# Optimization experiments

Measured on AMD Instinct MI355X. Metric: run time of the kernel, lower is better.

The kernel has to match this reference:

```python
import jax, jax.numpy as jnp
import numpy as np

EPSILON = 0.1  # adversarial perturbation magnitude (q = 1 norm)
N_HIDDEN1 = 4096


def setup_inputs() -> dict:
    key = jax.random.key(0)
    ks = jax.random.split(key, 6)
    batch, n_in, n_hid, n_out = 4096, 2048, N_HIDDEN1, 1024
    x = jax.random.normal(ks[0], (batch, n_in), dtype=jnp.float32)
    y = jax.random.normal(ks[1], (batch, n_out), dtype=jnp.float32)
    # AdvLinearNet params: beta ~ U[0,1)/sqrt(n_out), bias = 0
    beta = jax.random.uniform(ks[2], (n_in, n_out), dtype=jnp.float32) / np.sqrt(n_out)
    bias_lin = jnp.zeros((n_out,), dtype=jnp.float32)
    # AdvOneLayer params (gamma = 1.0): W1 = -U/ (gamma*n_hid), W2 = U/(gamma*n_out)
    W1 = -jax.random.uniform(ks[3], (n_hid, n_in), dtype=jnp.float32) / n_hid
    W2 = jax.random.uniform(ks[4], (n_out, n_hid), dtype=jnp.float32) / n_out
    bias1 = jnp.zeros((n_hid,), dtype=jnp.float32)
    bias2 = jnp.zeros((n_out,), dtype=jnp.float32)
    return {"x": x, "y": y, "beta": beta, "bias_lin": bias_lin,
            "W1": W1, "W2": W2, "bias1": bias1, "bias2": bias2, "adv": 1}


def reference(x, y, beta, bias_lin, W1, W2, bias1, bias2, adv):
    # ---- AdvLinearNet ----
    lin = jnp.matmul(x, beta) + bias_lin            # [B, n_out]
    if adv:
        # torch.norm(beta, dim=0, p=1) -> per-output-column L1 norm
        beta_norm = jnp.sum(jnp.abs(beta), axis=0)  # [n_out]
        lin = lin - EPSILON * y * beta_norm
    # ---- AdvOneLayer ----
    if adv:
        # Faithful to source: summand = W2[i, j] * n_hidden1 (the relu hidden
        # computation inside the double loop is dead code), so the adv output
        # is constant across the batch.
        one = N_HIDDEN1 * jnp.sum(W2, axis=1) + bias2      # [n_out]
        one = jnp.broadcast_to(one, lin.shape)             # [B, n_out]
    else:
        h = jax.nn.relu(jnp.matmul(x, W1.T) + bias1)       # [B, n_hid]
        one = jnp.matmul(h, W2.T) + bias2                  # [B, n_out]
    return lin + one
```

## Files before the change

kernel.cpp:

```cpp
#include <hip/hip_runtime.h>
#include <hip/hip_bf16.h>


typedef float    f32x4  __attribute__((ext_vector_type(4)));
typedef unsigned u32x4  __attribute__((ext_vector_type(4)));
typedef long     lx2    __attribute__((ext_vector_type(2)));

constexpr int M = 4096;
constexpr int N = 1024;
constexpr int K = 2048;
constexpr int NHID = 4096;

__device__ __forceinline__ unsigned pk4f8(float a, float b, float c, float d) {
    unsigned v = __builtin_amdgcn_cvt_pk_fp8_f32(a, b, 0, false);
    v = __builtin_amdgcn_cvt_pk_fp8_f32(c, d, v, true);
    return v;
}

__device__ __forceinline__ void gll16(const void* g, void* l) {
    __builtin_amdgcn_global_load_lds(
        (const __attribute__((address_space(1))) void*)g,
        (__attribute__((address_space(3))) void*)l, 16, 0, 0);
}

__global__ void __launch_bounds__(256) pre_kernel(
    const float* __restrict__ x, const float* __restrict__ beta,
    const float* __restrict__ W2,
    char* __restrict__ xb, char* __restrict__ bt,
    float* __restrict__ partials,
    float* __restrict__ wsum) {
    __shared__ float tls[64 * 132];
    const int bx = blockIdx.x, tid = threadIdx.x;
    if (bx < 1024) {
        const int rt = bx >> 4, kt = bx & 15;
        {
            const int r = tid >> 2, c0 = (tid & 3) * 32;
            const float* src = x + (size_t)(rt * 64 + r) * K + kt * 128 + c0;
            #pragma unroll
            for (int i = 0; i < 8; ++i)
                *(f32x4*)&tls[r * 132 + c0 + i * 4] = *(const f32x4*)(src + i * 4);
        }
        __syncthreads();
        {
            const int r = tid >> 2;
            const float* row = &tls[r * 132];
            char* orow = xb + (size_t)(rt * 64 + r) * K + kt * 128;
            #pragma unroll
            for (int uu = 0; uu < 2; ++uu) {
                const int u = (tid & 3) + uu * 4;
                const int p = u >> 2, q = u & 3;
                const float* h0 = row + p * 64 + q * 8;
                const float* h1 = h0 + 32;
                u32x4 o = { pk4f8(h0[0], h0[1], h0[2], h0[3]),
                            pk4f8(h0[4], h0[5], h0[6], h0[7]),
                            pk4f8(h1[0], h1[1], h1[2], h1[3]),
                            pk4f8(h1[4], h1[5], h1[6], h1[7]) };
                *(u32x4*)(orow + u * 16) = o;
            }
        }
    } else if (bx < 1536) {
        const int tile = bx - 1024, tk = tile & 31, tn = tile >> 5;
        {
            const int r = tid >> 2, c0 = (tid & 3) * 16;
            const float* src = beta + (size_t)(tk * 64 + r) * N + tn * 64 + c0;
            #pragma unroll
            for (int j = 0; j < 4; ++j)
                *(f32x4*)&tls[r * 68 + c0 + j * 4] = *(const f32x4*)(src + j * 4);
        }
        __syncthreads();
        {
            const int n = tid >> 2, q = tid & 3;
            float s = 0.f;
            float v0[8], v1[8];
            #pragma unroll
            for (int j = 0; j < 8; ++j) {
                v0[j] = tls[(q * 8 + j) * 68 + n];
                v1[j] = tls[(32 + q * 8 + j) * 68 + n];
                s += fabsf(v0[j]) + fabsf(v1[j]);
            }
            s += __shfl_xor(s, 1);
            s += __shfl_xor(s, 2);
            if (q == 0) partials[tk * 1024 + tn * 64 + n] = s;
            u32x4 o = { pk4f8(v0[0], v0[1], v0[2], v0[3]),
                        pk4f8(v0[4], v0[5], v0[6], v0[7]),
                        pk4f8(v1[0], v1[1], v1[2], v1[3]),
                        pk4f8(v1[4], v1[5], v1[6], v1[7]) };
            *(u32x4*)(bt + (size_t)(tn * 64 + n) * K + tk * 64 + q * 16) = o;
        }
    } else {
        const int b = bx - 1536;
        const int wv = tid >> 6, lane = tid & 63;
        const int row = b * 4 + wv;
        const f32x4* w4 = (const f32x4*)(W2 + (size_t)row * NHID);
        float acc = 0.f;
        #pragma unroll
        for (int i = 0; i < 16; ++i) {
            f32x4 v = w4[i * 64 + lane];
            acc += v[0] + v[1] + v[2] + v[3];
        }
        #pragma unroll
        for (int off = 32; off; off >>= 1) acc += __shfl_down(acc, off);
        if (lane == 0) wsum[row] = acc;
    }
}

constexpr int BKu = 128;
constexpr int NT  = K / BKu;
constexpr int ASZ = 128 * BKu;
constexpr int BSZ = 64 * BKu;

__global__ void __launch_bounds__(512, 4) gemm_kernel(
    const char* __restrict__ xb, const char* __restrict__ bt,
    const float* __restrict__ y,
    const float* __restrict__ partials, const float* __restrict__ wsum,
    const float* __restrict__ bias_lin, const float* __restrict__ bias2,
    float* __restrict__ out) {
    __shared__ __align__(16) char Al[3 * ASZ];
    __shared__ __align__(16) char Bl[3 * BSZ];

    const int tid = threadIdx.x, lane = tid & 63, w = tid >> 6;
    const int wm = w >> 1, wn = w & 1;
    const int c = blockIdx.x & 7, local = blockIdx.x >> 3;
    const int mb = ((c & 1) << 4) + (local >> 2);
    const int nb = ((c >> 1) << 2) + (local & 3);
    const int brow = mb * 128, bcol = nb * 64;

    const int srow = lane >> 3;
    const int sulog = (lane & 7) ^ srow;
    const char* asrc0 = xb + (size_t)(brow + w * 16 + srow) * K + sulog * 16;
    const char* asrc1 = asrc0 + (size_t)8 * K;
    const char* bsrc  = bt + (size_t)(bcol + w * 8 + srow) * K + sulog * 16;

    auto STAGE = [&](int buf, int t) {
        gll16(asrc0 + t * BKu, &Al[buf * ASZ + w * 2048]);
        gll16(asrc1 + t * BKu, &Al[buf * ASZ + w * 2048 + 1024]);
        gll16(bsrc  + t * BKu, &Bl[buf * BSZ + w * 1024]);
    };

    const int r = lane & 15, q = lane >> 4;
    int aoff[2][2], boff[2][2];
    #pragma unroll
    for (int m = 0; m < 2; ++m)
        #pragma unroll
        for (int p = 0; p < 2; ++p) {
            const int row = wm * 32 + m * 16 + r;
            aoff[m][p] = row * 128 + (((p * 4 + q) ^ (r & 7)) * 16);
        }
    #pragma unroll
    for (int n = 0; n < 2; ++n)
        #pragma unroll
        for (int p = 0; p < 2; ++p) {
            const int row = wn * 32 + n * 16 + r;
            boff[n][p] = row * 128 + (((p * 4 + q) ^ (r & 7)) * 16);
        }

    f32x4 acc[2][2];
    #pragma unroll
    for (int m = 0; m < 2; ++m)
        #pragma unroll
        for (int n = 0; n < 2; ++n) acc[m][n] = (f32x4)0.f;

    auto COMPUTE = [&](int buf) {
        const char* A = &Al[buf * ASZ];
        const char* B = &Bl[buf * BSZ];
        #pragma unroll
        for (int p = 0; p < 2; ++p) {
            lx2 a0 = *(const lx2*)&A[aoff[0][p]];
            lx2 a1 = *(const lx2*)&A[aoff[1][p]];
            lx2 b0 = *(const lx2*)&B[boff[0][p]];
            lx2 b1 = *(const lx2*)&B[boff[1][p]];
            acc[0][0] = __builtin_amdgcn_mfma_f32_16x16x32_fp8_fp8(a0.x, b0.x, acc[0][0], 0, 0, 0);
            acc[0][1] = __builtin_amdgcn_mfma_f32_16x16x32_fp8_fp8(a0.x, b1.x, acc[0][1], 0, 0, 0);
            acc[1][0] = __builtin_amdgcn_mfma_f32_16x16x32_fp8_fp8(a1.x, b0.x, acc[1][0], 0, 0, 0);
            acc[1][1] = __builtin_amdgcn_mfma_f32_16x16x32_fp8_fp8(a1.x, b1.x, acc[1][1], 0, 0, 0);
            acc[0][0] = __builtin_amdgcn_mfma_f32_16x16x32_fp8_fp8(a0.y, b0.y, acc[0][0], 0, 0, 0);
            acc[0][1] = __builtin_amdgcn_mfma_f32_16x16x32_fp8_fp8(a0.y, b1.y, acc[0][1], 0, 0, 0);
            acc[1][0] = __builtin_amdgcn_mfma_f32_16x16x32_fp8_fp8(a1.y, b0.y, acc[1][0], 0, 0, 0);
            acc[1][1] = __builtin_amdgcn_mfma_f32_16x16x32_fp8_fp8(a1.y, b1.y, acc[1][1], 0, 0, 0);
        }
    };

    STAGE(0, 0);
    STAGE(1, 1);
    for (int t = 0; t < NT; ++t) {
        if (t < NT - 1) { asm volatile("s_waitcnt vmcnt(3)" ::: "memory"); }
        else            { asm volatile("s_waitcnt vmcnt(0)" ::: "memory"); }
        __builtin_amdgcn_s_barrier();
        __builtin_amdgcn_sched_barrier(0);
        if (t + 2 < NT) STAGE((t + 2) % 3, t + 2);
        COMPUTE(t % 3);
    }

    #pragma unroll
    for (int n = 0; n < 2; ++n) {
        const int gc = bcol + wn * 32 + n * 16 + r;
        float bsum = 0.f;
        #pragma unroll 8
        for (int tk = 0; tk < 32; ++tk) bsum += partials[tk * 1024 + gc];
        const float be = 0.1f * bsum;
        const float ct = bias_lin[gc] + bias2[gc] + (float)NHID * wsum[gc];
        #pragma unroll
        for (int m = 0; m < 2; ++m) {
            const int gr0 = brow + wm * 32 + m * 16 + q * 4;
            f32x4 v = acc[m][n];
            #pragma unroll
            for (int rr = 0; rr < 4; ++rr) {
                size_t idx = (size_t)(gr0 + rr) * N + gc;
                out[idx] = v[rr] + ct - be * y[idx];
            }
        }
    }
}

extern "C" void kernel_launch(void* const* d_in, const int* in_sizes, int n_in,
                              void* d_out, int out_size, void* d_ws, size_t ws_size,
                              hipStream_t stream) {
    const float* x        = (const float*)d_in[0];
    const float* y        = (const float*)d_in[1];
    const float* beta     = (const float*)d_in[2];
    const float* bias_lin = (const float*)d_in[3];
    const float* W2       = (const float*)d_in[5];
    const float* bias2    = (const float*)d_in[7];
    float* out = (float*)d_out;

    float* partials = (float*)d_ws;
    float* wsum     = partials + 32 * 1024;
    char*  xb       = (char*)(wsum + 1024);
    char*  bts      = xb + (size_t)M * K;

    pre_kernel<<<1792, 256, 0, stream>>>(x, beta, W2, xb, bts, partials, wsum);
    gemm_kernel<<<512, 512, 0, stream>>>(xb, bts, y, partials, wsum,
                                         bias_lin, bias2, out);
}
```

Measured before the change: 36.08 us.

## Double-buffer LDS fragment reads in registers ahead of MFMA issue

Splits the compute step into a register-read phase and an MFMA phase. The next tile's A/B fragments are loaded from LDS into a second register set while the current set feeds the MFMAs, and the loop is fully unrolled. MFMA blocks are wrapped in s_setprio to favour matrix issue. The wait changes to vmcnt(0) every iteration, so the global prefetch effectively runs only one tile ahead. That can expose global-load latency, and the extra live fragment registers raise register pressure.

New measurement: 36.59 us. Within noise of the previous version (+1.4%).

```diff
diff --git a/kernel.cpp b/kernel.cpp
--- a/kernel.cpp
+++ b/kernel.cpp
@@ -160,15 +160,29 @@
         #pragma unroll
         for (int n = 0; n < 2; ++n) acc[m][n] = (f32x4)0.f;
 
-    auto COMPUTE = [&](int buf) {
+    lx2 Ar[2][2][2], Br[2][2][2];
+
+    auto RD = [&](int set, int buf) {
         const char* A = &Al[buf * ASZ];
         const char* B = &Bl[buf * BSZ];
         #pragma unroll
+        for (int m = 0; m < 2; ++m)
+            #pragma unroll
+            for (int p = 0; p < 2; ++p)
+                Ar[set][m][p] = *(const lx2*)&A[aoff[m][p]];
+        #pragma unroll
+        for (int n = 0; n < 2; ++n)
+            #pragma unroll
+            for (int p = 0; p < 2; ++p)
+                Br[set][n][p] = *(const lx2*)&B[boff[n][p]];
+    };
+
+    auto MM = [&](int set) {
+        __builtin_amdgcn_s_setprio(1);
+        #pragma unroll
         for (int p = 0; p < 2; ++p) {
-            lx2 a0 = *(const lx2*)&A[aoff[0][p]];
-            lx2 a1 = *(const lx2*)&A[aoff[1][p]];
-            lx2 b0 = *(const lx2*)&B[boff[0][p]];
-            lx2 b1 = *(const lx2*)&B[boff[1][p]];
+            lx2 a0 = Ar[set][0][p], a1 = Ar[set][1][p];
+            lx2 b0 = Br[set][0][p], b1 = Br[set][1][p];
             acc[0][0] = __builtin_amdgcn_mfma_f32_16x16x32_fp8_fp8(a0.x, b0.x, acc[0][0], 0, 0, 0);
             acc[0][1] = __builtin_amdgcn_mfma_f32_16x16x32_fp8_fp8(a0.x, b1.x, acc[0][1], 0, 0, 0);
             acc[1][0] = __builtin_amdgcn_mfma_f32_16x16x32_fp8_fp8(a1.x, b0.x, acc[1][0], 0, 0, 0);
@@ -178,17 +192,25 @@
             acc[1][0] = __builtin_amdgcn_mfma_f32_16x16x32_fp8_fp8(a1.y, b0.y, acc[1][0], 0, 0, 0);
             acc[1][1] = __builtin_amdgcn_mfma_f32_16x16x32_fp8_fp8(a1.y, b1.y, acc[1][1], 0, 0, 0);
         }
+        __builtin_amdgcn_s_setprio(0);
     };
 
     STAGE(0, 0);
     STAGE(1, 1);
+    asm volatile("s_waitcnt vmcnt(3)" ::: "memory");
+    __builtin_amdgcn_s_barrier();
+    __builtin_amdgcn_sched_barrier(0);
+    RD(0, 0);
+
+    #pragma unroll
     for (int t = 0; t < NT; ++t) {
-        if (t < NT - 1) { asm volatile("s_waitcnt vmcnt(3)" ::: "memory"); }
-        else            { asm volatile("s_waitcnt vmcnt(0)" ::: "memory"); }
+        asm volatile("s_waitcnt vmcnt(0)" ::: "memory");
         __builtin_amdgcn_s_barrier();
         __builtin_amdgcn_sched_barrier(0);
+        if (t + 1 < NT) RD((t + 1) % 2, (t + 1) % 3);
         if (t + 2 < NT) STAGE((t + 2) % 3, t + 2);
-        COMPUTE(t % 3);
+        __builtin_amdgcn_sched_barrier(0);
+        MM(t % 2);
     }
 
     #pragma unroll
```

## Switch GEMM to 32x32x16 FP8 MFMA with intra-block split-K across waves

Applied to the files above, without the earlier changes.

Replaces the 16x16x32 FP8 MFMA tiling with 32x32x16 MFMAs, so each wave computes a 64x32 tile over half of each K-tile. Two wave groups split K, and their partial accumulators are merged through LDS before the epilogue. The x and beta FP8 packing order is changed so the K layout matches the new MFMA operand ordering. Intended to cut LDS fragment loads and MFMA issue count per FLOP. In exchange it adds an LDS reduction with two extra barriers, and only half the waves run the epilogue.

Result: slower. 37.18 us (+3.1%).

```diff
diff --git a/kernel.cpp b/kernel.cpp
--- a/kernel.cpp
+++ b/kernel.cpp
@@ -3,6 +3,7 @@
 
 
 typedef float    f32x4  __attribute__((ext_vector_type(4)));
+typedef float    f32x16 __attribute__((ext_vector_type(16)));
 typedef unsigned u32x4  __attribute__((ext_vector_type(4)));
 typedef long     lx2    __attribute__((ext_vector_type(2)));
 
@@ -48,9 +49,9 @@
             #pragma unroll
             for (int uu = 0; uu < 2; ++uu) {
                 const int u = (tid & 3) + uu * 4;
-                const int p = u >> 2, q = u & 3;
-                const float* h0 = row + p * 64 + q * 8;
-                const float* h1 = h0 + 32;
+                const int j = u >> 1, h = u & 1;
+                const float* h0 = row + j * 32 + h * 8;
+                const float* h1 = h0 + 16;
                 u32x4 o = { pk4f8(h0[0], h0[1], h0[2], h0[3]),
                             pk4f8(h0[4], h0[5], h0[6], h0[7]),
                             pk4f8(h1[0], h1[1], h1[2], h1[3]),
@@ -70,13 +71,14 @@
         __syncthreads();
         {
             const int n = tid >> 2, q = tid & 3;
+            const int kb = (q >> 1) * 32 + (q & 1) * 8;
             float s = 0.f;
             float v0[8], v1[8];
             #pragma unroll
-            for (int j = 0; j < 8; ++j) {
-                v0[j] = tls[(q * 8 + j) * 68 + n];
-                v1[j] = tls[(32 + q * 8 + j) * 68 + n];
-                s += fabsf(v0[j]) + fabsf(v1[j]);
+            for (int jj = 0; jj < 8; ++jj) {
+                v0[jj] = tls[(kb + jj) * 68 + n];
+                v1[jj] = tls[(kb + 16 + jj) * 68 + n];
+                s += fabsf(v0[jj]) + fabsf(v1[jj]);
             }
             s += __shfl_xor(s, 1);
             s += __shfl_xor(s, 2);
@@ -119,7 +121,7 @@
     __shared__ __align__(16) char Bl[3 * BSZ];
 
     const int tid = threadIdx.x, lane = tid & 63, w = tid >> 6;
-    const int wm = w >> 1, wn = w & 1;
+    const int wk = w >> 2, wm = (w >> 1) & 1, wn = w & 1;
     const int c = blockIdx.x & 7, local = blockIdx.x >> 3;
     const int mb = ((c & 1) << 4) + (local >> 2);
     const int nb = ((c >> 1) << 2) + (local & 3);
@@ -137,46 +139,37 @@
         gll16(bsrc  + t * BKu, &Bl[buf * BSZ + w * 1024]);
     };
 
-    const int r = lane & 15, q = lane >> 4;
-    int aoff[2][2], boff[2][2];
+    const int rl = lane & 31, h = lane >> 5;
+    int aoff[2][2], boff[2];
     #pragma unroll
     for (int m = 0; m < 2; ++m)
         #pragma unroll
-        for (int p = 0; p < 2; ++p) {
-            const int row = wm * 32 + m * 16 + r;
-            aoff[m][p] = row * 128 + (((p * 4 + q) ^ (r & 7)) * 16);
+        for (int jj = 0; jj < 2; ++jj) {
+            const int j = wk * 2 + jj;
+            const int row = wm * 64 + m * 32 + rl;
+            aoff[m][jj] = row * 128 + (((2 * j + h) ^ (row & 7)) * 16);
         }
     #pragma unroll
-    for (int n = 0; n < 2; ++n)
-        #pragma unroll
-        for (int p = 0; p < 2; ++p) {
-            const int row = wn * 32 + n * 16 + r;
-            boff[n][p] = row * 128 + (((p * 4 + q) ^ (r & 7)) * 16);
-        }
-
-    f32x4 acc[2][2];
-    #pragma unroll
-    for (int m = 0; m < 2; ++m)
-        #pragma unroll
-        for (int n = 0; n < 2; ++n) acc[m][n] = (f32x4)0.f;
+    for (int jj = 0; jj < 2; ++jj) {
+        const int j = wk * 2 + jj;
+        const int row = wn * 32 + rl;
+        boff[jj] = row * 128 + (((2 * j + h) ^ (row & 7)) * 16);
+    }
+
+    f32x16 acc0 = (f32x16)0.f, acc1 = (f32x16)0.f;
 
     auto COMPUTE = [&](int buf) {
         const char* A = &Al[buf * ASZ];
         const char* B = &Bl[buf * BSZ];
         #pragma unroll
-        for (int p = 0; p < 2; ++p) {
-            lx2 a0 = *(const lx2*)&A[aoff[0][p]];
-            lx2 a1 = *(const lx2*)&A[aoff[1][p]];
-            lx2 b0 = *(const lx2*)&B[boff[0][p]];
-            lx2 b1 = *(const lx2*)&B[boff[1][p]];
-            acc[0][0] = __builtin_amdgcn_mfma_f32_16x16x32_fp8_fp8(a0.x, b0.x, acc[0][0], 0, 0, 0);
-            acc[0][1] = __builtin_amdgcn_mfma_f32_16x16x32_fp8_fp8(a0.x, b1.x, acc[0][1], 0, 0, 0);
-            acc[1][0] = __builtin_amdgcn_mfma_f32_16x16x32_fp8_fp8(a1.x, b0.x, acc[1][0], 0, 0, 0);
-            acc[1][1] = __builtin_amdgcn_mfma_f32_16x16x32_fp8_fp8(a1.x, b1.x, acc[1][1], 0, 0, 0);
-            acc[0][0] = __builtin_amdgcn_mfma_f32_16x16x32_fp8_fp8(a0.y, b0.y, acc[0][0], 0, 0, 0);
-            acc[0][1] = __builtin_amdgcn_mfma_f32_16x16x32_fp8_fp8(a0.y, b1.y, acc[0][1], 0, 0, 0);
-            acc[1][0] = __builtin_amdgcn_mfma_f32_16x16x32_fp8_fp8(a1.y, b0.y, acc[1][0], 0, 0, 0);
-            acc[1][1] = __builtin_amdgcn_mfma_f32_16x16x32_fp8_fp8(a1.y, b1.y, acc[1][1], 0, 0, 0);
+        for (int jj = 0; jj < 2; ++jj) {
+            lx2 a0 = *(const lx2*)&A[aoff[0][jj]];
+            lx2 a1 = *(const lx2*)&A[aoff[1][jj]];
+            lx2 b  = *(const lx2*)&B[boff[jj]];
+            acc0 = __builtin_amdgcn_mfma_f32_32x32x16_fp8_fp8(a0.x, b.x, acc0, 0, 0, 0);
+            acc1 = __builtin_amdgcn_mfma_f32_32x32x16_fp8_fp8(a1.x, b.x, acc1, 0, 0, 0);
+            acc0 = __builtin_amdgcn_mfma_f32_32x32x16_fp8_fp8(a0.y, b.y, acc0, 0, 0, 0);
+            acc1 = __builtin_amdgcn_mfma_f32_32x32x16_fp8_fp8(a1.y, b.y, acc1, 0, 0, 0);
         }
     };
 
@@ -191,9 +184,32 @@
         COMPUTE(t % 3);
     }
 
-    #pragma unroll
-    for (int n = 0; n < 2; ++n) {
-        const int gc = bcol + wn * 32 + n * 16 + r;
+    __syncthreads();
+    float* mrg = (float*)Al;
+    if (wk == 1) {
+        const int base = (w - 4) * 2048 + lane * 16;
+        #pragma unroll
+        for (int i = 0; i < 4; ++i) {
+            f32x4 v0 = { acc0[i * 4], acc0[i * 4 + 1], acc0[i * 4 + 2], acc0[i * 4 + 3] };
+            f32x4 v1 = { acc1[i * 4], acc1[i * 4 + 1], acc1[i * 4 + 2], acc1[i * 4 + 3] };
+            *(f32x4*)&mrg[base + i * 4]        = v0;
+            *(f32x4*)&mrg[base + 1024 + i * 4] = v1;
+        }
+    }
+    __syncthreads();
+    if (wk == 0) {
+        const int base = w * 2048 + lane * 16;
+        #pragma unroll
+        for (int i = 0; i < 4; ++i) {
+            f32x4 v0 = *(const f32x4*)&mrg[base + i * 4];
+            f32x4 v1 = *(const f32x4*)&mrg[base + 1024 + i * 4];
+            #pragma unroll
+            for (int e = 0; e < 4; ++e) {
+                acc0[i * 4 + e] += v0[e];
+                acc1[i * 4 + e] += v1[e];
+            }
+        }
+        const int gc = bcol + wn * 32 + rl;
         float bsum = 0.f;
         #pragma unroll 8
         for (int tk = 0; tk < 32; ++tk) bsum += partials[tk * 1024 + gc];
@@ -201,12 +217,16 @@
         const float ct = bias_lin[gc] + bias2[gc] + (float)NHID * wsum[gc];
         #pragma unroll
         for (int m = 0; m < 2; ++m) {
-            const int gr0 = brow + wm * 32 + m * 16 + q * 4;
-            f32x4 v = acc[m][n];
-            #pragma unroll
-            for (int rr = 0; rr < 4; ++rr) {
-                size_t idx = (size_t)(gr0 + rr) * N + gc;
-                out[idx] = v[rr] + ct - be * y[idx];
+            const int rbase = brow + wm * 64 + m * 32 + 4 * h;
+            #pragma unroll
+            for (int g = 0; g < 4; ++g) {
+                #pragma unroll
+                for (int jr = 0; jr < 4; ++jr) {
+                    const int row = rbase + g * 8 + jr;
+                    const size_t idx = (size_t)row * N + gc;
+                    const float a = (m == 0) ? acc0[g * 4 + jr] : acc1[g * 4 + jr];
+                    out[idx] = a + ct - be * y[idx];
+                }
             }
         }
     }
```

## Pre-swizzle fp8 operands into MFMA fragment layout and load directly to registers

Applied to the files above, without the earlier changes.

The pre-pass now writes x and beta in fp8 in a fragment-major layout that matches the 32x32x16 MFMA operand order, so each lane fetches its operands with one contiguous 16-byte global load. The GEMM drops shared-memory staging, barriers and swizzling, uses 32x32 MFMAs with a register prefetch depth of three, and has each wave compute a 64x32 tile. This removes LDS traffic and synchronisation, but gives up cross-wave data reuse through LDS, so redundant global/L2 reads rise. Latency hiding now rests on register prefetch alone.

After: 46.92 us. 1.3x slower.

```diff
diff --git a/kernel.cpp b/kernel.cpp
--- a/kernel.cpp
+++ b/kernel.cpp
@@ -3,6 +3,7 @@
 
 
 typedef float    f32x4  __attribute__((ext_vector_type(4)));
+typedef float    f32x16 __attribute__((ext_vector_type(16)));
 typedef unsigned u32x4  __attribute__((ext_vector_type(4)));
 typedef long     lx2    __attribute__((ext_vector_type(2)));
 
@@ -17,16 +18,10 @@
     return v;
 }
 
-__device__ __forceinline__ void gll16(const void* g, void* l) {
-    __builtin_amdgcn_global_load_lds(
-        (const __attribute__((address_space(1))) void*)g,
-        (__attribute__((address_space(3))) void*)l, 16, 0, 0);
-}
-
 __global__ void __launch_bounds__(256) pre_kernel(
     const float* __restrict__ x, const float* __restrict__ beta,
     const float* __restrict__ W2,
-    char* __restrict__ xb, char* __restrict__ bt,
+    char* __restrict__ xa, char* __restrict__ bt,
     float* __restrict__ partials,
     float* __restrict__ wsum) {
     __shared__ float tls[64 * 132];
@@ -42,21 +37,21 @@
         }
         __syncthreads();
         {
-            const int r = tid >> 2;
-            const float* row = &tls[r * 132];
-            char* orow = xb + (size_t)(rt * 64 + r) * K + kt * 128;
-            #pragma unroll
-            for (int uu = 0; uu < 2; ++uu) {
-                const int u = (tid & 3) + uu * 4;
-                const int p = u >> 2, q = u & 3;
-                const float* h0 = row + p * 64 + q * 8;
-                const float* h1 = h0 + 32;
-                u32x4 o = { pk4f8(h0[0], h0[1], h0[2], h0[3]),
-                            pk4f8(h0[4], h0[5], h0[6], h0[7]),
-                            pk4f8(h1[0], h1[1], h1[2], h1[3]),
-                            pk4f8(h1[4], h1[5], h1[6], h1[7]) };
-                *(u32x4*)(orow + u * 16) = o;
-            }
+            const int f = tid >> 5, lp = tid & 31;
+            const int mtL = f >> 2, ksL = f & 3;
+            const float* fr = &tls[(mtL * 32 + lp) * 132 + ksL * 32];
+            const size_t fbase =
+                ((size_t)(rt * 2 + mtL) * 64 + (kt * 4 + ksL)) * 1024;
+            u32x4 o0 = { pk4f8(fr[0],  fr[1],  fr[2],  fr[3]),
+                         pk4f8(fr[4],  fr[5],  fr[6],  fr[7]),
+                         pk4f8(fr[16], fr[17], fr[18], fr[19]),
+                         pk4f8(fr[20], fr[21], fr[22], fr[23]) };
+            u32x4 o1 = { pk4f8(fr[8],  fr[9],  fr[10], fr[11]),
+                         pk4f8(fr[12], fr[13], fr[14], fr[15]),
+                         pk4f8(fr[24], fr[25], fr[26], fr[27]),
+                         pk4f8(fr[28], fr[29], fr[30], fr[31]) };
+            *(u32x4*)(xa + fbase + lp * 16)        = o0;
+            *(u32x4*)(xa + fbase + (lp + 32) * 16) = o1;
         }
     } else if (bx < 1536) {
         const int tile = bx - 1024, tk = tile & 31, tn = tile >> 5;
@@ -69,23 +64,29 @@
         }
         __syncthreads();
         {
-            const int n = tid >> 2, q = tid & 3;
+            const int f = tid >> 6, l = tid & 63;
+            const int nt_f = f >> 1, ks_f = f & 1;
+            const int nl = l & 31, h = l >> 5;
+            const int nloc = nt_f * 32 + nl;
+            const int kb = ks_f * 32 + h * 8;
+            float v0[8], v1[8];
             float s = 0.f;
-            float v0[8], v1[8];
             #pragma unroll
             for (int j = 0; j < 8; ++j) {
-                v0[j] = tls[(q * 8 + j) * 68 + n];
-                v1[j] = tls[(32 + q * 8 + j) * 68 + n];
+                v0[j] = tls[(kb + j) * 68 + nloc];
+                v1[j] = tls[(kb + 16 + j) * 68 + nloc];
                 s += fabsf(v0[j]) + fabsf(v1[j]);
             }
-            s += __shfl_xor(s, 1);
-            s += __shfl_xor(s, 2);
-            if (q == 0) partials[tk * 1024 + tn * 64 + n] = s;
+            s += __shfl_xor(s, 32);
+            if (nl == l)
+                partials[(tk * 2 + ks_f) * 1024 + tn * 64 + nloc] = s;
             u32x4 o = { pk4f8(v0[0], v0[1], v0[2], v0[3]),
                         pk4f8(v0[4], v0[5], v0[6], v0[7]),
                         pk4f8(v1[0], v1[1], v1[2], v1[3]),
                         pk4f8(v1[4], v1[5], v1[6], v1[7]) };
-            *(u32x4*)(bt + (size_t)(tn * 64 + n) * K + tk * 64 + q * 16) = o;
+            const size_t fbase =
+                ((size_t)(tn * 2 + nt_f) * 64 + (tk * 2 + ks_f)) * 1024;
+            *(u32x4*)(bt + fbase + l * 16) = o;
         }
     } else {
         const int b = bx - 1536;
@@ -104,109 +105,61 @@
     }
 }
 
-constexpr int BKu = 128;
-constexpr int NT  = K / BKu;
-constexpr int ASZ = 128 * BKu;
-constexpr int BSZ = 64 * BKu;
-
-__global__ void __launch_bounds__(512, 4) gemm_kernel(
-    const char* __restrict__ xb, const char* __restrict__ bt,
+__global__ void __launch_bounds__(256, 2) gemm_kernel(
+    const char* __restrict__ xa, const char* __restrict__ bt,
     const float* __restrict__ y,
     const float* __restrict__ partials, const float* __restrict__ wsum,
     const float* __restrict__ bias_lin, const float* __restrict__ bias2,
     float* __restrict__ out) {
-    __shared__ __align__(16) char Al[3 * ASZ];
-    __shared__ __align__(16) char Bl[3 * BSZ];
+    const int tid = threadIdx.x, lane = tid & 63, w = tid >> 6;
+    const int c = blockIdx.x & 7, local = blockIdx.x >> 3;
+    const int a = c * 8 + (local >> 3);
+    const int b = (local & 7) * 4 + w;
 
-    const int tid = threadIdx.x, lane = tid & 63, w = tid >> 6;
-    const int wm = w >> 1, wn = w & 1;
-    const int c = blockIdx.x & 7, local = blockIdx.x >> 3;
-    const int mb = ((c & 1) << 4) + (local >> 2);
-    const int nb = ((c >> 1) << 2) + (local & 3);
-    const int brow = mb * 128, bcol = nb * 64;
+    const char* a0p = xa + ((size_t)(2 * a) * 64) * 1024 + lane * 16;
+    const char* a1p = a0p + 64 * 1024;
+    const char* bp  = bt + ((size_t)b * 64) * 1024 + lane * 16;
 
-    const int srow = lane >> 3;
-    const int sulog = (lane & 7) ^ srow;
-    const char* asrc0 = xb + (size_t)(brow + w * 16 + srow) * K + sulog * 16;
-    const char* asrc1 = asrc0 + (size_t)8 * K;
-    const char* bsrc  = bt + (size_t)(bcol + w * 8 + srow) * K + sulog * 16;
+    f32x16 acc0 = (f32x16)0.f, acc1 = (f32x16)0.f;
 
-    auto STAGE = [&](int buf, int t) {
-        gll16(asrc0 + t * BKu, &Al[buf * ASZ + w * 2048]);
-        gll16(asrc1 + t * BKu, &Al[buf * ASZ + w * 2048 + 1024]);
-        gll16(bsrc  + t * BKu, &Bl[buf * BSZ + w * 1024]);
-    };
+    lx2 A0[4], A1[4], Bf[4];
+    #define LDSET(s, ks)                                            \
+        A0[s] = *(const lx2*)(a0p + (ks) * 1024);                   \
+        A1[s] = *(const lx2*)(a1p + (ks) * 1024);                   \
+        Bf[s] = *(const lx2*)(bp  + (ks) * 1024);
 
-    const int r = lane & 15, q = lane >> 4;
-    int aoff[2][2], boff[2][2];
+    LDSET(0, 0)
+    LDSET(1, 1)
+    LDSET(2, 2)
     #pragma unroll
-    for (int m = 0; m < 2; ++m)
+    for (int ks = 0; ks < 64; ++ks) {
+        const int s = ks & 3;
+        if (ks + 3 < 64) { LDSET((ks + 3) & 3, ks + 3) }
+        acc0 = __builtin_amdgcn_mfma_f32_32x32x16_fp8_fp8(A0[s].x, Bf[s].x, acc0, 0, 0, 0);
+        acc1 = __builtin_amdgcn_mfma_f32_32x32x16_fp8_fp8(A1[s].x, Bf[s].x, acc1, 0, 0, 0);
+        acc0 = __builtin_amdgcn_mfma_f32_32x32x16_fp8_fp8(A0[s].y, Bf[s].y, acc0, 0, 0, 0);
+        acc1 = __builtin_amdgcn_mfma_f32_32x32x16_fp8_fp8(A1[s].y, Bf[s].y, acc1, 0, 0, 0);
+    }
+    #undef LDSET
+
+    const int rl = lane & 31, h = lane >> 5;
+    const int gc = b * 32 + rl;
+    float bsum = 0.f;
+    #pragma unroll 8
+    for (int p = 0; p < 64; ++p) bsum += partials[p * 1024 + gc];
+    const float be = 0.1f * bsum;
+    const float ct = bias_lin[gc] + bias2[gc] + (float)NHID * wsum[gc];
+    #pragma unroll
+    for (int m = 0; m < 2; ++m) {
+        const int rbase = a * 64 + m * 32 + 4 * h;
         #pragma unroll
-        for (int p = 0; p < 2; ++p) {
-            const int row = wm * 32 + m * 16 + r;
-            aoff[m][p] = row * 128 + (((p * 4 + q) ^ (r & 7)) * 16);
-        }
-    #pragma unroll
-    for (int n = 0; n < 2; ++n)
-        #pragma unroll
-        for (int p = 0; p < 2; ++p) {
-            const int row = wn * 32 + n * 16 + r;
-            boff[n][p] = row * 128 + (((p * 4 + q) ^ (r & 7)) * 16);
-        }
-
-    f32x4 acc[2][2];
-    #pragma unroll
-    for (int m = 0; m < 2; ++m)
-        #pragma unroll
-        for (int n = 0; n < 2; ++n) acc[m][n] = (f32x4)0.f;
-
-    auto COMPUTE = [&](int buf) {
-        const char* A = &Al[buf * ASZ];
-        const char* B = &Bl[buf * BSZ];
-        #pragma unroll
-        for (int p = 0; p < 2; ++p) {
-            lx2 a0 = *(const lx2*)&A[aoff[0][p]];
-            lx2 a1 = *(const lx2*)&A[aoff[1][p]];
-            lx2 b0 = *(const lx2*)&B[boff[0][p]];
-            lx2 b1 = *(const lx2*)&B[boff[1][p]];
-            acc[0][0] = __builtin_amdgcn_mfma_f32_16x16x32_fp8_fp8(a0.x, b0.x, acc[0][0], 0, 0, 0);
-            acc[0][1] = __builtin_amdgcn_mfma_f32_16x16x32_fp8_fp8(a0.x, b1.x, acc[0][1], 0, 0, 0);
-            acc[1][0] = __builtin_amdgcn_mfma_f32_16x16x32_fp8_fp8(a1.x, b0.x, acc[1][0], 0, 0, 0);
-            acc[1][1] = __builtin_amdgcn_mfma_f32_16x16x32_fp8_fp8(a1.x, b1.x, acc[1][1], 0, 0, 0);
-            acc[0][0] = __builtin_amdgcn_mfma_f32_16x16x32_fp8_fp8(a0.y, b0.y, acc[0][0], 0, 0, 0);
-            acc[0][1] = __builtin_amdgcn_mfma_f32_16x16x32_fp8_fp8(a0.y, b1.y, acc[0][1], 0, 0, 0);
-            acc[1][0] = __builtin_amdgcn_mfma_f32_16x16x32_fp8_fp8(a1.y, b0.y, acc[1][0], 0, 0, 0);
-            acc[1][1] = __builtin_amdgcn_mfma_f32_16x16x32_fp8_fp8(a1.y, b1.y, acc[1][1], 0, 0, 0);
-        }
-    };
-
-    STAGE(0, 0);
-    STAGE(1, 1);
-    for (int t = 0; t < NT; ++t) {
-        if (t < NT - 1) { asm volatile("s_waitcnt vmcnt(3)" ::: "memory"); }
-        else            { asm volatile("s_waitcnt vmcnt(0)" ::: "memory"); }
-        __builtin_amdgcn_s_barrier();
-        __builtin_amdgcn_sched_barrier(0);
-        if (t + 2 < NT) STAGE((t + 2) % 3, t + 2);
-        COMPUTE(t % 3);
-    }
-
-    #pragma unroll
-    for (int n = 0; n < 2; ++n) {
-        const int gc = bcol + wn * 32 + n * 16 + r;
-        float bsum = 0.f;
-        #pragma unroll 8
-        for (int tk = 0; tk < 32; ++tk) bsum += partials[tk * 1024 + gc];
-        const float be = 0.1f * bsum;
-        const float ct = bias_lin[gc] + bias2[gc] + (float)NHID * wsum[gc];
-        #pragma unroll
-        for (int m = 0; m < 2; ++m) {
-            const int gr0 = brow + wm * 32 + m * 16 + q * 4;
-            f32x4 v = acc[m][n];
+        for (int g = 0; g < 4; ++g) {
             #pragma unroll
-            for (int rr = 0; rr < 4; ++rr) {
-                size_t idx = (size_t)(gr0 + rr) * N + gc;
-                out[idx] = v[rr] + ct - be * y[idx];
+            for (int jr = 0; jr < 4; ++jr) {
+                const int row = rbase + g * 8 + jr;
+                const size_t idx = (size_t)row * N + gc;
+                const float av = (m == 0) ? acc0[g * 4 + jr] : acc1[g * 4 + jr];
+                out[idx] = av + ct - be * y[idx];
             }
         }
     }
@@ -224,11 +177,11 @@
     float* out = (float*)d_out;
 
     float* partials = (float*)d_ws;
-    float* wsum     = partials + 32 * 1024;
-    char*  xb       = (char*)(wsum + 1024);
-    char*  bts      = xb + (size_t)M * K;
+    float* wsum     = partials + 64 * 1024;
+    char*  xa       = (char*)(wsum + 1024);
+    char*  bts      = xa + (size_t)M * K;
 
-    pre_kernel<<<1792, 256, 0, stream>>>(x, beta, W2, xb, bts, partials, wsum);
-    gemm_kernel<<<512, 512, 0, stream>>>(xb, bts, y, partials, wsum,
+    pre_kernel<<<1792, 256, 0, stream>>>(x, beta, W2, xa, bts, partials, wsum);
+    gemm_kernel<<<512, 256, 0, stream>>>(xa, bts, y, partials, wsum,
                                          bias_lin, bias2, out);
 }
```
